# Performance work log

Hardware: AMD Instinct MI355X
Metric: run time of the kernel (lower is better)

Reference implementation:

```python
import math
import jax, jax.numpy as jnp
import numpy as np

B, S, HID, NH = 8, 512, 1024, 16
D = HID // NH          # head dim = 64
SPAN = 512             # att_span = max_relative_positions = max_position_embeddings


def _linear(x, W, b):
    # torch nn.Linear: y = x @ W.T + b, W is [out, in]
    return jnp.einsum('...i,oi->...o', x, W) + b


def _heads(x):
    # [B, S, HID] -> [B, NH, S, D]
    b, s, _ = x.shape
    return x.reshape(b, s, NH, D).transpose(0, 2, 1, 3)


def setup_inputs() -> dict:
    key = jax.random.key(0)
    ks = jax.random.split(key, 16)
    f = lambda i, shape, sc=1.0: jax.random.normal(ks[i], shape, dtype=jnp.float32) * sc
    return {
        'q': f(0, (B, S, HID)),
        'k': f(1, (B, S, HID)),
        'v': f(2, (B, S, HID)),
        'attention_mask': jnp.tril(jnp.ones((S, S), dtype=bool))[None, None],  # causal [1,1,S,S]
        'Wq': f(3, (HID, HID), 0.02), 'bq': jnp.zeros((HID,), jnp.float32),
        'Wk': f(4, (HID, HID), 0.02), 'bk': jnp.zeros((HID,), jnp.float32),
        'Wv': f(5, (HID, HID), 0.02), 'bv': jnp.zeros((HID,), jnp.float32),
        'Wpk': f(6, (HID, HID), 0.02), 'bpk': jnp.zeros((HID,), jnp.float32),
        'Wpq': f(7, (HID, HID), 0.02), 'bpq': jnp.zeros((HID,), jnp.float32),
        'rel_emb': f(8, (2 * SPAN, HID), 0.02),
    }


def reference(q, k, v, attention_mask, Wq, bq, Wk, bk, Wv, bv, Wpk, bpk, Wpq, bpq, rel_emb):
    scale_factor = 3  # 1 (content) + c2p + p2c
    scale = 1.0 / math.sqrt(D * scale_factor)

    ql = _heads(_linear(q, Wq, bq))   # [B,NH,S,D]
    kl = _heads(_linear(k, Wk, bk))
    vl = _heads(_linear(v, Wv, bv))

    # content-to-content scores
    scores = jnp.einsum('bhqd,bhkd->bhqk', ql, kl) * scale

    # relative positions (no bucketing since position_buckets = -1)
    rel = jnp.arange(S)[:, None] - jnp.arange(S)[None, :]          # [S,S]
    c2p_pos = jnp.clip(rel + SPAN, 0, 2 * SPAN - 1)
    p2c_pos = jnp.clip(-rel + SPAN, 0, 2 * SPAN - 1)

    # projected relative-position embeddings -> [NH, 2*SPAN, D]
    pk = _linear(rel_emb, Wpk, bpk).reshape(2 * SPAN, NH, D).transpose(1, 0, 2)
    pq = _linear(rel_emb, Wpq, bpq).reshape(2 * SPAN, NH, D).transpose(1, 0, 2)

    # content-to-position: out[b,h,q,k] = (q . pos_key)[b,h,q, c2p_pos[q,k]]
    c2p = jnp.einsum('bhqd,hjd->bhqj', ql, pk) * scale             # [B,NH,S,2*SPAN]
    c2p = jnp.take_along_axis(c2p, jnp.broadcast_to(c2p_pos[None, None], (B, NH, S, S)), axis=-1)

    # position-to-content: gathered[b,h,k,q] = (k . pos_query)[b,h,k, p2c_pos[k,q]], then transpose
    p2c = jnp.einsum('bhkd,hjd->bhkj', kl, pq) * scale             # [B,NH,S,2*SPAN]
    p2c = jnp.take_along_axis(p2c, jnp.broadcast_to(p2c_pos[None, None], (B, NH, S, S)), axis=-1)

    scores = scores + c2p + jnp.swapaxes(p2c, -1, -2)
    # subtract detached row max (as in torch: .max(...).values.detach())
    scores = scores - jax.lax.stop_gradient(scores.max(axis=-1, keepdims=True))

    # XSoftmax: masked softmax, then zero masked positions
    neg = jnp.float32(-1e30)
    probs = jax.nn.softmax(jnp.where(attention_mask, scores, neg), axis=-1)
    probs = jnp.where(attention_mask, probs, 0.0)

    ctx = jnp.einsum('bhqk,bhkd->bhqd', probs, vl)                 # [B,NH,S,D]
    return ctx.transpose(0, 2, 1, 3).reshape(B, S, HID)
```

## Files before the change

kernel.cpp:

```cpp
#include <hip/hip_runtime.h>
#include <hip/hip_bf16.h>
#include <math.h>

#define SCALE 0.07216878364870323f
#define NEG_BIG -1e30f

typedef __attribute__((ext_vector_type(8))) short bf16x8;
typedef __attribute__((ext_vector_type(4))) short bf16x4;
typedef __attribute__((ext_vector_type(4))) float f32x4;
#define MFMA_BF16 __builtin_amdgcn_mfma_f32_16x16x32_bf16

#define BARX()   asm volatile("s_barrier" ::: "memory")
#define VMCNT2() asm volatile("s_waitcnt vmcnt(2)" ::: "memory")
#define VMCNT0() asm volatile("s_waitcnt vmcnt(0)" ::: "memory")

static __device__ __forceinline__ float bf2f(__hip_bfloat16 x) { return __bfloat162float(x); }
static __device__ __forceinline__ __hip_bfloat16 f2bf(float x) { return __float2bfloat16(x); }
static __device__ __forceinline__ short f2bs(float x) {
  union { __hip_bfloat16 b; short s; } u; u.b = __float2bfloat16(x); return u.s;
}
static __device__ __forceinline__ float s2f(short v) {
  union { float f; unsigned u; } x; x.u = ((unsigned)(unsigned short)v) << 16; return x.f;
}
static __device__ __forceinline__ bf16x4 cvt4(float4 f) {
  bf16x4 r; r[0] = f2bs(f.x); r[1] = f2bs(f.y); r[2] = f2bs(f.z); r[3] = f2bs(f.w);
  return r;
}
static __device__ __forceinline__ bf16x8 ldg8(const __hip_bfloat16* p) {
  return *(const bf16x8*)p;
}
static __device__ __forceinline__ void gl_lds16(const __hip_bfloat16* g, __hip_bfloat16* l) {
  __builtin_amdgcn_global_load_lds(
      (const __attribute__((address_space(1))) void*)g,
      (__attribute__((address_space(3))) void*)l, 16, 0, 0);
}

struct CvtJob { const float* src; __hip_bfloat16* dst; int n4; };
struct CvtArgs { CvtJob j[9]; };

__global__ __launch_bounds__(256) void cvt_kernel(CvtArgs a) {
  const CvtJob jb = a.j[blockIdx.y];
  const float4* s = (const float4*)jb.src;
  bf16x4* d = (bf16x4*)jb.dst;
  const int stride = gridDim.x * 256;
  for (int i = blockIdx.x * 256 + threadIdx.x; i < jb.n4; i += stride)
    d[i] = cvt4(s[i]);
}

struct Gemm { const __hip_bfloat16* A; const __hip_bfloat16* W;
              const float* bias; __hip_bfloat16* out; int mode; int mBits; int nBlk;
              float oscale; };
struct ProjArgs { Gemm g[5]; };

static __device__ __forceinline__ void stage_half(const __hip_bfloat16* gtile,
                                                  __hip_bfloat16* ltile,
                                                  int half, int wave, int lane) {
  const int r = lane >> 3;
  const int chunk = (lane & 7) ^ r;
#pragma unroll
  for (int c = 0; c < 2; c++) {
    const int rowbase = half * 128 + c * 64 + wave * 8;
    gl_lds16(gtile + (size_t)(rowbase + r) * 1024 + chunk * 8,
             ltile + (size_t)rowbase * 64);
  }
}

__global__ __launch_bounds__(512, 2) void proj_kernel(ProjArgs pa) {
  const Gemm g = pa.g[blockIdx.y];
  if ((int)blockIdx.x >= g.nBlk) return;
  __shared__ __hip_bfloat16 As[2][256][64];
  __shared__ __hip_bfloat16 Ws[2][256][64];

  const int bid = blockIdx.x;
  const int m0 = (bid & ((1 << g.mBits) - 1)) * 256;
  const int n0 = (bid >> g.mBits) * 256;
  const int tid = threadIdx.x;
  const int wave = tid >> 6, lane = tid & 63;
  const int q16 = lane >> 4, l16 = lane & 15;
  const int wr = wave >> 2, wc = wave & 3;
  const int l7 = l16 & 7;

  const __hip_bfloat16* Ag = g.A + (size_t)m0 * 1024;
  const __hip_bfloat16* Wg = g.W + (size_t)n0 * 1024;

  f32x4 acc[8][4] = {};

  stage_half(Ag, &As[0][0][0], 0, wave, lane);
  stage_half(Ag, &As[0][0][0], 1, wave, lane);
  stage_half(Wg, &Ws[0][0][0], 0, wave, lane);
  stage_half(Wg, &Ws[0][0][0], 1, wave, lane);
  stage_half(Ag + 64, &As[1][0][0], 0, wave, lane);
  VMCNT2();
  BARX();

  for (int t = 0; t < 16; ++t) {
    const int cur = t & 1;
    const __hip_bfloat16* Ac = &As[cur][0][0];
    const __hip_bfloat16* Wc = &Ws[cur][0][0];
    __hip_bfloat16* An = &As[cur ^ 1][0][0];
    __hip_bfloat16* Wn = &Ws[cur ^ 1][0][0];
    const __hip_bfloat16* gAn = Ag + (size_t)(t + 1) * 64;
    const __hip_bfloat16* gWn = Wg + (size_t)(t + 1) * 64;
    const bool pf = (t + 1 < 16);

#pragma unroll
    for (int kh = 0; kh < 2; kh++) {
      const int csw = ((kh * 4 + q16) ^ l7) * 8;
      bf16x8 bw[4];
#pragma unroll
      for (int ni = 0; ni < 4; ni++)
        bw[ni] = *(const bf16x8*)(Wc + (size_t)(wc * 64 + ni * 16 + l16) * 64 + csw);
#pragma unroll
      for (int mh = 0; mh < 2; mh++) {
        bf16x8 af[4];
#pragma unroll
        for (int mi = 0; mi < 4; mi++)
          af[mi] = *(const bf16x8*)(Ac + (size_t)(wr * 128 + mh * 64 + mi * 16 + l16) * 64 + csw);
        const int ph = kh * 2 + mh;
        if (pf) {
          if (ph == 0)      stage_half(gAn, An, 1, wave, lane);
          else if (ph == 1) stage_half(gWn, Wn, 0, wave, lane);
          else if (ph == 2) stage_half(gWn, Wn, 1, wave, lane);
        }
        __builtin_amdgcn_s_setprio(1);
#pragma unroll
        for (int ni = 0; ni < 4; ni++)
#pragma unroll
          for (int mi = 0; mi < 4; mi++)
            acc[mh * 4 + mi][ni] =
                MFMA_BF16(af[mi], bw[ni], acc[mh * 4 + mi][ni], 0, 0, 0);
        __builtin_amdgcn_s_setprio(0);
      }
    }
    BARX();
    if (t + 2 < 16) {
      stage_half(Ag + (size_t)(t + 2) * 64, &As[cur][0][0], 0, wave, lane);
      VMCNT2();
    } else {
      VMCNT0();
    }
    BARX();
  }

#pragma unroll
  for (int ni = 0; ni < 4; ni++) {
    const int n = n0 + wc * 64 + ni * 16 + l16;
#pragma unroll
    for (int mi = 0; mi < 8; mi++) {
#pragma unroll
      for (int rr = 0; rr < 4; rr++) {
        const int m = m0 + wr * 128 + mi * 16 + q16 * 4 + rr;
        float val = acc[mi][ni][rr];
        size_t oidx;
        if (g.mode == 0) {
          val = (val + g.bias[n]) * g.oscale;
          const int b = m >> 9, s = m & 511;
          const int h = n >> 6, d = n & 63;
          oidx = ((size_t)((b * 16 + h) * 512 + s)) * 64 + d;
        } else if (g.mode == 1) {
          val = (val + g.bias[m]) * g.oscale;
          const int b = n >> 9, s = n & 511;
          const int h = m >> 6, d = m & 63;
          oidx = ((size_t)((b * 16 + h) * 64 + d)) * 512 + s;
        } else {
          val = (val + g.bias[n]) * g.oscale;
          const int h = n >> 6, d = n & 63;
          oidx = ((size_t)(h * 512 + m)) * 64 + d;
        }
        g.out[oidx] = f2bf(val);
      }
    }
  }
}

__global__ __launch_bounds__(256) void attn_kernel(
    const __hip_bfloat16* __restrict__ ql,
    const __hip_bfloat16* __restrict__ kl,
    const __hip_bfloat16* __restrict__ vlT,
    const __hip_bfloat16* __restrict__ pk,
    const __hip_bfloat16* __restrict__ pq,
    float* __restrict__ out)
{
  __shared__ __align__(16) __hip_bfloat16 pool[2][64][72];
  __shared__ __align__(16) __hip_bfloat16 pqs[2][32][72];
  __shared__ __align__(16) float qkbuf[32][36];
  __shared__ __align__(16) __hip_bfloat16 cpb[2][32][68];
  __shared__ __align__(16) __hip_bfloat16 pT[64][36];
  __shared__ __align__(16) __hip_bfloat16 sc[32][528];
  __shared__ float mred[32];
  __shared__ float rowsum[32];

  const int bid = blockIdx.x;
  const int qt = 15 - (bid >> 7);
  const int bh = bid & 127;
  const int h = bh & 15, b = bh >> 4;
  const int q0 = qt * 32;

  const __hip_bfloat16* qlp = ql + (size_t)bh * 512 * 64;
  const __hip_bfloat16* klp = kl + (size_t)bh * 512 * 64;
  const __hip_bfloat16* vtp = vlT + (size_t)bh * 64 * 512;
  const __hip_bfloat16* pkp = pk + (size_t)h * 512 * 64;
  const __hip_bfloat16* pqp = pq + (size_t)h * 512 * 64;

  const int tid = threadIdx.x, wave = tid >> 6, lane = tid & 63;
  const int q16 = lane >> 4, l16 = lane & 15;
  const int wr = wave & 1, wc = wave >> 1;

  bf16x8 qlB[2][2];
#pragma unroll
  for (int ksi = 0; ksi < 2; ksi++)
#pragma unroll
    for (int bq = 0; bq < 2; bq++)
      qlB[ksi][bq] = ldg8(qlp + (size_t)(q0 + bq * 16 + l16) * 64 + ksi * 32 + q16 * 8);

  {
    int4 z = {0, 0, 0, 0};
    *(int4*)(&pqs[1][tid >> 3][(tid & 7) * 8]) = z;
  }

  const int kEnd = q0 + 32;
  const int nIter = kEnd >> 5;

  const int sr = tid >> 3, sseg = tid & 7;
  int4 rKv, rPKv, rPQv;
  {
    rKv  = ((const int4*)(klp + (size_t)(q0 + sr) * 64))[sseg];
    rPKv = ((const int4*)(pkp + (size_t)(0 + sr) * 64))[sseg];
    rPQv = ((const int4*)(pqp + (size_t)(0 + sr) * 64))[sseg];
  }

  const int aq = tid >> 3;
  const int kb = (tid & 7) * 4;
  float mloc = NEG_BIG;

  for (int it = 0; it < nIter; ++it) {
    const int k0 = q0 - it * 32;
    const int par = it & 1;
    *(int4*)(&pool[par][sr][sseg * 8])      = rKv;
    *(int4*)(&pool[par][32 + sr][sseg * 8]) = rPKv;
    *(int4*)(&pqs[par][sr][sseg * 8])       = rPQv;
    __syncthreads();

    const int arb = (wave == 1) ? 32 : 0;
    f32x4 a4[2][2] = {};
    __builtin_amdgcn_s_setprio(1);
#pragma unroll
    for (int ksi = 0; ksi < 2; ksi++) {
      const int ko = ksi * 32 + q16 * 8;
      bf16x8 Af0 = *(const bf16x8*)(&pool[par][arb + l16][ko]);
      bf16x8 Af1 = *(const bf16x8*)(&pool[par][arb + 16 + l16][ko]);
      bf16x8 Bf0, Bf1;
      if (wave < 2) {
        Bf0 = qlB[ksi][0];
        Bf1 = qlB[ksi][1];
      } else {
        const int ps = (wave == 2) ? (par ^ 1) : par;
        Bf0 = *(const bf16x8*)(&pqs[ps][l16][ko]);
        Bf1 = *(const bf16x8*)(&pqs[ps][16 + l16][ko]);
      }
      a4[0][0] = MFMA_BF16(Af0, Bf0, a4[0][0], 0, 0, 0);
      a4[0][1] = MFMA_BF16(Af0, Bf1, a4[0][1], 0, 0, 0);
      a4[1][0] = MFMA_BF16(Af1, Bf0, a4[1][0], 0, 0, 0);
      a4[1][1] = MFMA_BF16(Af1, Bf1, a4[1][1], 0, 0, 0);
    }
    __builtin_amdgcn_s_setprio(0);

    if (wave == 0) {
#pragma unroll
      for (int a = 0; a < 2; a++)
#pragma unroll
        for (int bq = 0; bq < 2; bq++)
          *(f32x4*)(&qkbuf[bq * 16 + l16][a * 16 + q16 * 4]) = a4[a][bq];
    } else if (wave == 1) {
#pragma unroll
      for (int a = 0; a < 2; a++)
#pragma unroll
        for (int bq = 0; bq < 2; bq++) {
          bf16x4 v;
#pragma unroll
          for (int r = 0; r < 4; r++) v[r] = f2bs(a4[a][bq][r]);
          const int q = bq * 16 + l16, jr = a * 16 + q16 * 4;
          *(bf16x4*)(&cpb[par][q][32 + jr]) = v;
          *(bf16x4*)(&cpb[par ^ 1][q][jr]) = v;
        }
    } else {
      const int rb = (wave == 3) ? 32 : 0;
#pragma unroll
      for (int a = 0; a < 2; a++)
#pragma unroll
        for (int bq = 0; bq < 2; bq++) {
          bf16x4 v;
#pragma unroll
          for (int r = 0; r < 4; r++) v[r] = f2bs(a4[a][bq][r]);
          *(bf16x4*)(&pT[rb + bq * 16 + l16][a * 16 + q16 * 4]) = v;
        }
    }
    __syncthreads();

    if (it + 1 < nIter) {
      const int k0n = k0 - 32, jbn = (it + 1) * 32;
      rKv  = ((const int4*)(klp + (size_t)(k0n + sr) * 64))[sseg];
      rPKv = ((const int4*)(pkp + (size_t)(jbn + sr) * 64))[sseg];
      rPQv = ((const int4*)(pqp + (size_t)(jbn + sr) * 64))[sseg];
    }

    {
      const f32x4 qk4 = *(const f32x4*)(&qkbuf[aq][kb]);
      bf16x4 scv;
#pragma unroll
      for (int j = 0; j < 4; j++) {
        const int kl_ = kb + j;
        const int dlt = aq - kl_;
        const float v = qk4[j] + bf2f(cpb[par][aq][dlt + 32])
                               + bf2f(pT[dlt + 32][kl_]);
        const bool msk = (it == 0) && (dlt < 0);
        if (!msk) mloc = fmaxf(mloc, v);
        scv[j] = msk ? f2bs(NEG_BIG) : f2bs(v);
      }
      *(bf16x4*)(&sc[aq][k0 + kb]) = scv;
    }
  }

  {
    float m = mloc;
    m = fmaxf(m, __shfl_xor(m, 1));
    m = fmaxf(m, __shfl_xor(m, 2));
    m = fmaxf(m, __shfl_xor(m, 4));
    if ((tid & 7) == 0) mred[aq] = m;
  }
  __syncthreads();

  {
    const int row = tid >> 3, sub = tid & 7;
    const float m = mred[row];
    float s = 0.f;
    for (int c = sub * 8; c < kEnd; c += 64) {
      bf16x8 x8 = *(const bf16x8*)(&sc[row][c]);
      bf16x8 p8;
#pragma unroll
      for (int e = 0; e < 8; e++) {
        const float p = __expf(s2f(x8[e]) - m);
        p8[e] = f2bs(p);
        s += p;
      }
      *(bf16x8*)(&sc[row][c]) = p8;
    }
    for (int off = 1; off < 8; off <<= 1) s += __shfl_xor(s, off);
    if (sub == 0) rowsum[row] = s;
  }

  f32x4 octx[2] = {};
  {
    int p = 0;
    for (int k0 = 0; k0 < kEnd; k0 += 64, p ^= 1) {
      {
        const int r = tid >> 2, seg = tid & 3;
        const int4* src = (const int4*)(vtp + (size_t)r * 512 + k0);
        *(int4*)(&pool[p][r][seg * 8])       = src[seg];
        *(int4*)(&pool[p][r][(seg + 4) * 8]) = src[seg + 4];
      }
      __syncthreads();
      __builtin_amdgcn_s_setprio(1);
#pragma unroll
      for (int sub = 0; sub < 2; sub++) {
        const int kk = k0 + sub * 32;
        if (kk < kEnd) {
          bf16x8 af = *(const bf16x8*)(&sc[wr * 16 + l16][kk + q16 * 8]);
#pragma unroll
          for (int cs = 0; cs < 2; cs++) {
            bf16x8 bv = *(const bf16x8*)(&pool[p][wc * 32 + cs * 16 + l16][sub * 32 + q16 * 8]);
            octx[cs] = MFMA_BF16(af, bv, octx[cs], 0, 0, 0);
          }
        }
      }
      __builtin_amdgcn_s_setprio(0);
    }
  }

  for (int cs = 0; cs < 2; cs++) {
    const int d = wc * 32 + cs * 16 + l16;
    for (int rr = 0; rr < 4; rr++) {
      const int qh = wr * 16 + q16 * 4 + rr;
      const float val = octx[cs][rr] / rowsum[qh];
      out[((size_t)(b * 512 + q0 + qh)) * 1024 + h * 64 + d] = val;
    }
  }
}

extern "C" void kernel_launch(void* const* d_in, const int* in_sizes, int n_in,
                              void* d_out, int out_size, void* d_ws, size_t ws_size,
                              hipStream_t stream) {
  const float* q   = (const float*)d_in[0];
  const float* k   = (const float*)d_in[1];
  const float* v   = (const float*)d_in[2];
  const float* Wq  = (const float*)d_in[4];
  const float* bq  = (const float*)d_in[5];
  const float* Wk  = (const float*)d_in[6];
  const float* bk  = (const float*)d_in[7];
  const float* Wv  = (const float*)d_in[8];
  const float* bv  = (const float*)d_in[9];
  const float* Wpk = (const float*)d_in[10];
  const float* bpk = (const float*)d_in[11];
  const float* Wpq = (const float*)d_in[12];
  const float* bpq = (const float*)d_in[13];
  const float* rel = (const float*)d_in[14];
  float* out = (float*)d_out;

  char* ws = (char*)d_ws;
  const size_t MB = 1u << 20;
  __hip_bfloat16* bqi  = (__hip_bfloat16*)(ws);
  __hip_bfloat16* bki  = (__hip_bfloat16*)(ws + 8 * MB);
  __hip_bfloat16* bvi  = (__hip_bfloat16*)(ws + 16 * MB);
  __hip_bfloat16* bWq  = (__hip_bfloat16*)(ws + 24 * MB);
  __hip_bfloat16* bWk  = (__hip_bfloat16*)(ws + 26 * MB);
  __hip_bfloat16* bWv  = (__hip_bfloat16*)(ws + 28 * MB);
  __hip_bfloat16* bWpk = (__hip_bfloat16*)(ws + 30 * MB);
  __hip_bfloat16* bWpq = (__hip_bfloat16*)(ws + 32 * MB);
  __hip_bfloat16* brel = (__hip_bfloat16*)(ws + 34 * MB);
  __hip_bfloat16* wql  = (__hip_bfloat16*)(ws + 35 * MB);
  __hip_bfloat16* wkl  = (__hip_bfloat16*)(ws + 43 * MB);
  __hip_bfloat16* wvlT = (__hip_bfloat16*)(ws + 51 * MB);
  __hip_bfloat16* wpk  = (__hip_bfloat16*)(ws + 59 * MB);
  __hip_bfloat16* wpq  = (__hip_bfloat16*)(ws + 60 * MB);

  CvtArgs ca;
  ca.j[0] = { q,   bqi,  4194304 / 4 };
  ca.j[1] = { k,   bki,  4194304 / 4 };
  ca.j[2] = { v,   bvi,  4194304 / 4 };
  ca.j[3] = { Wq,  bWq,  1048576 / 4 };
  ca.j[4] = { Wk,  bWk,  1048576 / 4 };
  ca.j[5] = { Wv,  bWv,  1048576 / 4 };
  ca.j[6] = { Wpk, bWpk, 1048576 / 4 };
  ca.j[7] = { Wpq, bWpq, 1048576 / 4 };
  ca.j[8] = { rel + (size_t)512 * 1024, brel, 524288 / 4 };
  cvt_kernel<<<dim3(1024, 9), 256, 0, stream>>>(ca);

  ProjArgs pj;
  pj.g[0] = { bqi,  bWq,  bq,  wql,  0, 4, 64, SCALE };
  pj.g[1] = { bki,  bWk,  bk,  wkl,  0, 4, 64, 1.0f };
  pj.g[2] = { bWv,  bvi,  bv,  wvlT, 1, 2, 64, 1.0f };
  pj.g[3] = { brel, bWpk, bpk, wpk,  2, 1, 8,  1.0f };
  pj.g[4] = { brel, bWpq, bpq, wpq,  2, 1, 8,  SCALE };
  proj_kernel<<<dim3(64, 5), 512, 0, stream>>>(pj);

  attn_kernel<<<2048, 256, 0, stream>>>(wql, wkl, wvlT, wpk, wpq, out);
}
```

Baseline: 245.6 us.

## Fuse PV into score loop with online softmax, drop full score buffer

Replaces the stored 32x512 bf16 score row buffer and the separate softmax and PV passes with an online-softmax scheme. Each 32-key tile's probabilities are rescaled by a running max and immediately multiplied with a V^T tile loaded in the same iteration. The next K/PK/PQ global loads are also issued before the first barrier instead of after the second. This removes about 33KB of LDS, which could raise occupancy, and removes the second loop over keys. In exchange it adds an extra barrier, an exp and a rescale of the accumulators every iteration, and exp(0)=1 handling for fully masked rows depends on using -INFINITY carefully.

```diff
diff --git a/kernel.cpp b/kernel.cpp
--- a/kernel.cpp
+++ b/kernel.cpp
@@ -186,9 +186,10 @@
   __shared__ __align__(16) float qkbuf[32][36];
   __shared__ __align__(16) __hip_bfloat16 cpb[2][32][68];
   __shared__ __align__(16) __hip_bfloat16 pT[64][36];
-  __shared__ __align__(16) __hip_bfloat16 sc[32][528];
+  __shared__ __align__(16) __hip_bfloat16 ptile[32][40];
+  __shared__ __align__(16) __hip_bfloat16 vt[64][40];
   __shared__ float mred[32];
-  __shared__ float rowsum[32];
+  __shared__ float rsum[32];
 
   const int bid = blockIdx.x;
   const int qt = 15 - (bid >> 7);
@@ -222,16 +223,19 @@
   const int nIter = kEnd >> 5;
 
   const int sr = tid >> 3, sseg = tid & 7;
-  int4 rKv, rPKv, rPQv;
+  const int vr = tid >> 2, vs = tid & 3;
+  int4 rKv, rPKv, rPQv, rVt;
   {
     rKv  = ((const int4*)(klp + (size_t)(q0 + sr) * 64))[sseg];
     rPKv = ((const int4*)(pkp + (size_t)(0 + sr) * 64))[sseg];
     rPQv = ((const int4*)(pqp + (size_t)(0 + sr) * 64))[sseg];
+    rVt  = ((const int4*)(vtp + (size_t)vr * 512 + q0))[vs];
   }
 
   const int aq = tid >> 3;
   const int kb = (tid & 7) * 4;
-  float mloc = NEG_BIG;
+  float m_old = -INFINITY, s_part = 0.f;
+  f32x4 octx[2] = {};
 
   for (int it = 0; it < nIter; ++it) {
     const int k0 = q0 - it * 32;
@@ -239,6 +243,12 @@
     *(int4*)(&pool[par][sr][sseg * 8])      = rKv;
     *(int4*)(&pool[par][32 + sr][sseg * 8]) = rPKv;
     *(int4*)(&pqs[par][sr][sseg * 8])       = rPQv;
+    if (it + 1 < nIter) {
+      const int k0n = k0 - 32, jbn = (it + 1) * 32;
+      rKv  = ((const int4*)(klp + (size_t)(k0n + sr) * 64))[sseg];
+      rPKv = ((const int4*)(pkp + (size_t)(jbn + sr) * 64))[sseg];
+      rPQv = ((const int4*)(pqp + (size_t)(jbn + sr) * 64))[sseg];
+    }
     __syncthreads();
 
     const int arb = (wave == 1) ? 32 : 0;
@@ -264,7 +274,6 @@
       a4[1][1] = MFMA_BF16(Af1, Bf1, a4[1][1], 0, 0, 0);
     }
     __builtin_amdgcn_s_setprio(0);
-
     if (wave == 0) {
 #pragma unroll
       for (int a = 0; a < 2; a++)
@@ -297,91 +306,74 @@
     }
     __syncthreads();
 
-    if (it + 1 < nIter) {
-      const int k0n = k0 - 32, jbn = (it + 1) * 32;
-      rKv  = ((const int4*)(klp + (size_t)(k0n + sr) * 64))[sseg];
-      rPKv = ((const int4*)(pkp + (size_t)(jbn + sr) * 64))[sseg];
-      rPQv = ((const int4*)(pqp + (size_t)(jbn + sr) * 64))[sseg];
-    }
-
     {
       const f32x4 qk4 = *(const f32x4*)(&qkbuf[aq][kb]);
-      bf16x4 scv;
+      float v[4];
+      float tmax = -INFINITY;
 #pragma unroll
       for (int j = 0; j < 4; j++) {
-        const int kl_ = kb + j;
-        const int dlt = aq - kl_;
-        const float v = qk4[j] + bf2f(cpb[par][aq][dlt + 32])
-                               + bf2f(pT[dlt + 32][kl_]);
-        const bool msk = (it == 0) && (dlt < 0);
-        if (!msk) mloc = fmaxf(mloc, v);
-        scv[j] = msk ? f2bs(NEG_BIG) : f2bs(v);
-      }
-      *(bf16x4*)(&sc[aq][k0 + kb]) = scv;
+        const int dlt = aq - (kb + j);
+        v[j] = qk4[j] + bf2f(cpb[par][aq][dlt + 32]) + bf2f(pT[dlt + 32][kb + j]);
+        if ((it == 0) && (dlt < 0)) v[j] = -INFINITY;
+        else tmax = fmaxf(tmax, v[j]);
+      }
+      tmax = fmaxf(tmax, __shfl_xor(tmax, 1));
+      tmax = fmaxf(tmax, __shfl_xor(tmax, 2));
+      tmax = fmaxf(tmax, __shfl_xor(tmax, 4));
+      const float m_new = fmaxf(m_old, tmax);
+      const float f = __expf(m_old - m_new);
+      bf16x4 pv4;
+      float psum = 0.f;
+#pragma unroll
+      for (int j = 0; j < 4; j++) {
+        const float p = __expf(v[j] - m_new);
+        pv4[j] = f2bs(p);
+        psum += p;
+      }
+      s_part = s_part * f + psum;
+      m_old = m_new;
+      *(bf16x4*)(&ptile[aq][kb]) = pv4;
+      if ((tid & 7) == 0) mred[aq] = f;
+    }
+    {
+      *(int4*)(&vt[vr][vs * 8]) = rVt;
+      if (it + 1 < nIter)
+        rVt = ((const int4*)(vtp + (size_t)vr * 512 + (k0 - 32)))[vs];
+    }
+    __syncthreads();
+
+    {
+      float fr[4];
+#pragma unroll
+      for (int rr = 0; rr < 4; rr++) fr[rr] = mred[wr * 16 + q16 * 4 + rr];
+      bf16x8 af = *(const bf16x8*)(&ptile[wr * 16 + l16][q16 * 8]);
+      __builtin_amdgcn_s_setprio(1);
+#pragma unroll
+      for (int cs = 0; cs < 2; cs++) {
+        bf16x8 bv = *(const bf16x8*)(&vt[wc * 32 + cs * 16 + l16][q16 * 8]);
+        f32x4 c = octx[cs];
+#pragma unroll
+        for (int rr = 0; rr < 4; rr++) c[rr] *= fr[rr];
+        octx[cs] = MFMA_BF16(af, bv, c, 0, 0, 0);
+      }
+      __builtin_amdgcn_s_setprio(0);
     }
   }
 
   {
-    float m = mloc;
-    m = fmaxf(m, __shfl_xor(m, 1));
-    m = fmaxf(m, __shfl_xor(m, 2));
-    m = fmaxf(m, __shfl_xor(m, 4));
-    if ((tid & 7) == 0) mred[aq] = m;
+    float s = s_part;
+    s += __shfl_xor(s, 1);
+    s += __shfl_xor(s, 2);
+    s += __shfl_xor(s, 4);
+    if ((tid & 7) == 0) rsum[aq] = s;
   }
   __syncthreads();
-
-  {
-    const int row = tid >> 3, sub = tid & 7;
-    const float m = mred[row];
-    float s = 0.f;
-    for (int c = sub * 8; c < kEnd; c += 64) {
-      bf16x8 x8 = *(const bf16x8*)(&sc[row][c]);
-      bf16x8 p8;
-#pragma unroll
-      for (int e = 0; e < 8; e++) {
-        const float p = __expf(s2f(x8[e]) - m);
-        p8[e] = f2bs(p);
-        s += p;
-      }
-      *(bf16x8*)(&sc[row][c]) = p8;
-    }
-    for (int off = 1; off < 8; off <<= 1) s += __shfl_xor(s, off);
-    if (sub == 0) rowsum[row] = s;
-  }
-
-  f32x4 octx[2] = {};
-  {
-    int p = 0;
-    for (int k0 = 0; k0 < kEnd; k0 += 64, p ^= 1) {
-      {
-        const int r = tid >> 2, seg = tid & 3;
-        const int4* src = (const int4*)(vtp + (size_t)r * 512 + k0);
-        *(int4*)(&pool[p][r][seg * 8])       = src[seg];
-        *(int4*)(&pool[p][r][(seg + 4) * 8]) = src[seg + 4];
-      }
-      __syncthreads();
-      __builtin_amdgcn_s_setprio(1);
-#pragma unroll
-      for (int sub = 0; sub < 2; sub++) {
-        const int kk = k0 + sub * 32;
-        if (kk < kEnd) {
-          bf16x8 af = *(const bf16x8*)(&sc[wr * 16 + l16][kk + q16 * 8]);
-#pragma unroll
-          for (int cs = 0; cs < 2; cs++) {
-            bf16x8 bv = *(const bf16x8*)(&pool[p][wc * 32 + cs * 16 + l16][sub * 32 + q16 * 8]);
-            octx[cs] = MFMA_BF16(af, bv, octx[cs], 0, 0, 0);
-          }
-        }
-      }
-      __builtin_amdgcn_s_setprio(0);
-    }
-  }
 
   for (int cs = 0; cs < 2; cs++) {
     const int d = wc * 32 + cs * 16 + l16;
     for (int rr = 0; rr < 4; rr++) {
       const int qh = wr * 16 + q16 * 4 + rr;
-      const float val = octx[cs][rr] / rowsum[qh];
+      const float val = octx[cs][rr] / rsum[qh];
       out[((size_t)(b * 512 + q0 + qh)) * 1024 + h * 64 + d] = val;
     }
   }
```

Result: faster. 231.5 us (-5.7%).
